# Optimization experiments

Hardware: AMD Instinct MI355X
Metric: run time of the kernel (lower is better)

Reference implementation:

```python
import jax, jax.numpy as jnp
import numpy as np

N = 100000
E = 500000
D_IN = 128
D_H = 128
MAX_ITERS = 3  # min(int(T=2.0)+1, 3); step weights all >= 0.5 so no early break


def setup_inputs() -> dict:
    key = jax.random.key(0)
    ks = jax.random.split(key, 7)
    node_feats = jax.random.normal(ks[0], (N, D_IN), dtype=jnp.float32)
    edge_index = jax.random.randint(ks[1], (2, E), 0, N, dtype=jnp.int64)
    init = lambda k, shp, fan: jax.random.normal(k, shp, dtype=jnp.float32) / np.float32(np.sqrt(fan))
    W_s = init(ks[2], (D_H, D_IN), D_IN)        # Linear(d_in, d_h, bias=False)
    W_pc = init(ks[3], (D_H, D_H), D_H)         # Linear(d_h, d_h, bias=False)
    W_edge = init(ks[4], (D_H, 2 * D_H), 2 * D_H)  # Linear(2*d_h, d_h, bias=False)
    W_gate_w = init(ks[5], (1, 2 * D_H), 2 * D_H)  # Linear(2*d_h, 1)
    W_gate_b = jnp.zeros((1,), jnp.float32)
    T = jnp.float32(2.0)  # learnable iteration-count parameter, init tree_iterations
    return dict(node_feats=node_feats, edge_index=edge_index, W_s=W_s, W_pc=W_pc,
                W_edge=W_edge, W_gate_w=W_gate_w, W_gate_b=W_gate_b, T=T)


def _step(h, p_idx, c_idx, W_pc, W_edge, W_gate_w, W_gate_b):
    h_p = h[p_idx]                                   # [E, d_h] gather
    h_c = h[c_idx]                                   # [E, d_h] gather
    ec = jnp.concatenate([h_p, h_c], axis=1)         # [E, 2*d_h]
    msg = ec @ W_edge.T                              # edge projection
    alpha = jax.nn.sigmoid(ec @ W_gate_w.T + W_gate_b)  # [E, 1] gate
    msg = msg * alpha
    # scatter_add into both endpoints (symmetric aggregation)
    agg = jnp.zeros_like(h).at[p_idx].add(msg).at[c_idx].add(msg)
    new_h = jax.nn.relu(agg @ W_pc.T + h)
    return new_h + h  # residual=True


def reference(node_feats, edge_index, W_s, W_pc, W_edge, W_gate_w, W_gate_b, T):
    p_idx, c_idx = edge_index[0], edge_index[1]
    h = node_feats @ W_s.T                           # [N, d_h]
    for step in range(MAX_ITERS):
        w = jax.nn.sigmoid(T - step)                 # learned step weight
        step_h = _step(h, p_idx, c_idx, W_pc, W_edge, W_gate_w, W_gate_b)
        h = h + w * (step_h - h)
    return h  # outputs['hidden'] (dropout is identity in eval)
```

## Files before the change

### kernel.cpp

```cpp
#include <hip/hip_runtime.h>
#include <cstdio>
#include <cstddef>

#define DH 128

typedef _Float16 f16;
typedef __attribute__((ext_vector_type(8))) _Float16 f16x8;
typedef __attribute__((ext_vector_type(4))) _Float16 f16x4;
typedef __attribute__((ext_vector_type(2))) _Float16 f16x2;
typedef __attribute__((ext_vector_type(4))) float    f32x4;
typedef unsigned int u32;

__global__ __launch_bounds__(128) void prep2(const float* __restrict__ Wpc,
                                             const float* __restrict__ Wedge,
                                             const float* __restrict__ Ws,
                                             f16* __restrict__ Bg16,
                                             f16* __restrict__ Ws16,
                                             const int* __restrict__ idx,
                                             int* __restrict__ cnt, int twoE)
{
    int o = blockIdx.x;
    int k = threadIdx.x;
    if (o < 256) {
        int orow = o & 127;
        int col  = (o < 128) ? k : (128 + k);
        float acc = 0.f;
        for (int m = 0; m < 128; ++m)
            acc += Wpc[orow * 128 + m] * Wedge[m * 256 + col];
        Bg16[o * 128 + k] = (f16)acc;
    } else if (o < 384) {
        int row = o - 256;
        Ws16[row * 128 + k] = (f16)Ws[row * 128 + k];
    } else {
        const int stride = (gridDim.x - 384) * 128;
        for (int i = (o - 384) * 128 + k; i < twoE; i += stride)
            atomicAdd(cnt + idx[i], 1);
    }
}

template<int OUT, int NT, bool AF32, bool WF32, bool WF16, bool FUSES>
__global__ __launch_bounds__(256) void mfma_gemm_t(const void* __restrict__ Avp,
                                                   const f16* __restrict__ B16,
                                                   float* __restrict__ Cf,
                                                   f16* __restrict__ Ch,
                                                   const float* __restrict__ wg,
                                                   float* __restrict__ s,
                                                   int M)
{
    const int lane = threadIdx.x & 63;
    const int row0 = blockIdx.x * (NT * 64) + (threadIdx.x >> 6) * (NT * 16);
    const int r = lane & 15, kg = lane >> 4;

    int  mrow[NT];
    bool ok[NT];
    f16x8 a[NT][4];
#pragma unroll
    for (int t = 0; t < NT; ++t) {
        mrow[t] = row0 + t * 16 + r;
        ok[t]   = (mrow[t] < M);
        int ar  = ok[t] ? mrow[t] : M - 1;
        if constexpr (AF32) {
            const float4* Ap = (const float4*)((const float*)Avp + (size_t)ar * 128);
#pragma unroll
            for (int q = 0; q < 4; ++q) {
                float4 f0 = Ap[kg * 2 + q * 8];
                float4 f1 = Ap[kg * 2 + q * 8 + 1];
                f16x8 fr = {(f16)f0.x, (f16)f0.y, (f16)f0.z, (f16)f0.w,
                            (f16)f1.x, (f16)f1.y, (f16)f1.z, (f16)f1.w};
                a[t][q] = fr;
            }
        } else {
            const f16x8* Ap = (const f16x8*)((const f16*)Avp + (size_t)ar * 128 + kg * 8);
            a[t][0] = Ap[0]; a[t][1] = Ap[4]; a[t][2] = Ap[8]; a[t][3] = Ap[12];
        }
    }

    float sp0[NT], sp1[NT];
    if constexpr (FUSES) {
#pragma unroll
        for (int t = 0; t < NT; ++t) { sp0[t] = 0.f; sp1[t] = 0.f; }
    }

    for (int ct = 0; ct < OUT / 16; ++ct) {
        const f16x8* Bp = (const f16x8*)(B16 + (size_t)(ct * 16 + r) * 128 + kg * 8);
        f16x8 b0 = Bp[0], b1 = Bp[4], b2 = Bp[8], b3 = Bp[12];
        const int o0 = ct * 16 + kg * 4;
        float w0, w1, w2, w3, u0, u1, u2, u3;
        if constexpr (FUSES) {
            w0 = wg[o0]; w1 = wg[o0+1]; w2 = wg[o0+2]; w3 = wg[o0+3];
            u0 = wg[128+o0]; u1 = wg[128+o0+1]; u2 = wg[128+o0+2]; u3 = wg[128+o0+3];
        }
#pragma unroll
        for (int t = 0; t < NT; ++t) {
            f32x4 acc = {0.f, 0.f, 0.f, 0.f};
            acc = __builtin_amdgcn_mfma_f32_16x16x32_f16(b0, a[t][0], acc, 0, 0, 0);
            acc = __builtin_amdgcn_mfma_f32_16x16x32_f16(b1, a[t][1], acc, 0, 0, 0);
            acc = __builtin_amdgcn_mfma_f32_16x16x32_f16(b2, a[t][2], acc, 0, 0, 0);
            acc = __builtin_amdgcn_mfma_f32_16x16x32_f16(b3, a[t][3], acc, 0, 0, 0);
            if (ok[t]) {
                if constexpr (WF32)
                    *(float4*)(Cf + (size_t)mrow[t] * OUT + o0) =
                        make_float4(acc[0], acc[1], acc[2], acc[3]);
                if constexpr (WF16) {
                    f16x4 hv = {(f16)acc[0], (f16)acc[1], (f16)acc[2], (f16)acc[3]};
                    *(f16x4*)(Ch + (size_t)mrow[t] * OUT + o0) = hv;
                }
            }
            if constexpr (FUSES) {
                sp0[t] += acc[0]*w0 + acc[1]*w1 + acc[2]*w2 + acc[3]*w3;
                sp1[t] += acc[0]*u0 + acc[1]*u1 + acc[2]*u2 + acc[3]*u3;
            }
        }
    }
    if constexpr (FUSES) {
#pragma unroll
        for (int t = 0; t < NT; ++t) {
            float p0 = sp0[t], p1 = sp1[t];
            p0 += __shfl_xor(p0, 16); p0 += __shfl_xor(p0, 32);
            p1 += __shfl_xor(p1, 16); p1 += __shfl_xor(p1, 32);
            if (kg == 0 && ok[t])
                *(float2*)(s + 2 * mrow[t]) = make_float2(p0, p1);
        }
    }
}

#define SCAN_B 256
__global__ __launch_bounds__(SCAN_B) void scan1(const int* __restrict__ cnt,
                                                int* __restrict__ bsum, int Nn)
{
    __shared__ int sm[SCAN_B];
    int i = blockIdx.x * SCAN_B + threadIdx.x;
    sm[threadIdx.x] = (i < Nn) ? cnt[i] : 0;
    __syncthreads();
    for (int off = SCAN_B / 2; off > 0; off >>= 1) {
        if (threadIdx.x < off) sm[threadIdx.x] += sm[threadIdx.x + off];
        __syncthreads();
    }
    if (threadIdx.x == 0) bsum[blockIdx.x] = sm[0];
}

__global__ __launch_bounds__(1024) void scan2(int* __restrict__ bsum, int nb,
                                              int* __restrict__ totalOut)
{
    __shared__ int sm[1024];
    int t = threadIdx.x;
    sm[t] = (t < nb) ? bsum[t] : 0;
    __syncthreads();
    for (int off = 1; off < 1024; off <<= 1) {
        int u = (t >= off) ? sm[t - off] : 0;
        __syncthreads();
        sm[t] += u;
        __syncthreads();
    }
    if (t < nb) bsum[t] = (t == 0) ? 0 : sm[t - 1];
    if (t == nb - 1) *totalOut = sm[t];
}

__global__ __launch_bounds__(SCAN_B) void scan3(const int* __restrict__ cnt,
                                                const int* __restrict__ bsum,
                                                int* __restrict__ base,
                                                int* __restrict__ cursor, int Nn)
{
    __shared__ int sm[SCAN_B];
    int i = blockIdx.x * SCAN_B + threadIdx.x;
    int v = (i < Nn) ? cnt[i] : 0;
    sm[threadIdx.x] = v;
    __syncthreads();
    for (int off = 1; off < SCAN_B; off <<= 1) {
        int u = (threadIdx.x >= off) ? sm[threadIdx.x - off] : 0;
        __syncthreads();
        sm[threadIdx.x] += u;
        __syncthreads();
    }
    if (i < Nn) {
        int b = bsum[blockIdx.x] + sm[threadIdx.x] - v;
        base[i] = b;
        cursor[i] = b;
    }
}

__global__ __launch_bounds__(256) void fill_xcd(const int* __restrict__ idx,
                                                int* __restrict__ cursor,
                                                int* __restrict__ adjp,
                                                int E, int Nn)
{
    const int xcd  = blockIdx.x & 7;
    const int gblk = blockIdx.x >> 3;
    const int ngrp = gridDim.x >> 3;
    const int twoE = 2 * E;
    const int lo = xcd * Nn, hi = lo + Nn;
    for (int i = gblk * blockDim.x + threadIdx.x; i < twoE; i += ngrp * blockDim.x) {
        int node = idx[i];
        int n8 = node << 3;
        if (n8 < lo || n8 >= hi) continue;
        int side  = (i >= E);
        int e     = side ? i - E : i;
        int other = side ? idx[e] : idx[E + e];
        int pos = atomicAdd(cursor + node, 1);
        adjp[pos] = other | (side << 31);
    }
}

template<bool LAST>
__global__ __launch_bounds__(256) void agg8(const f16* __restrict__ g16,
                                            const int* __restrict__ adjp,
                                            const int* __restrict__ base,
                                            const float* __restrict__ sIn,
                                            float* __restrict__ sOut,
                                            float* __restrict__ hOut,
                                            f16* __restrict__ h16,
                                            const float* __restrict__ wg,
                                            const float* __restrict__ gbp,
                                            const float* __restrict__ Tp,
                                            float stepf, int Nn, int twoE)
{
    const int lane = threadIdx.x & 63;
    const int grp  = lane >> 4;
    const int gl   = lane & 15;
    const int wvid = (blockIdx.x * blockDim.x + threadIdx.x) >> 6;
    int n = wvid * 4 + grp;
    const bool nOK = (n < Nn);
    if (n >= Nn) n = Nn - 1;
    const float gb = gbp[0];
    const float w  = 1.f / (1.f + expf(-(Tp[0] - stepf)));
    const int b0 = base[n], b1 = base[n + 1];
    const int deg = b1 - b0;
    const float s1n = sIn[2 * n], s2n = sIn[2 * n + 1];
    const int d0 = gl << 3;

    f16x8 o1 = *(const f16x8*)(g16 + (size_t)n * 256 + d0);
    f16x8 o2 = *(const f16x8*)(g16 + (size_t)n * 256 + 128 + d0);
    f16x8 hv16 = *(const f16x8*)(h16 + (size_t)n * DH + d0);

    f16x2 acc0 = {(f16)0.f, (f16)0.f};
    f16x2 acc1 = {(f16)0.f, (f16)0.f};
    f16x2 acc2 = {(f16)0.f, (f16)0.f};
    f16x2 acc3 = {(f16)0.f, (f16)0.f};
    float aPl = 0.f, aCl = 0.f;

    union V8 { f16x8 v; f16x2 h2[4]; };
    union AU { u32 w; f16x2 h; unsigned short us[2]; };

    int t = 0;
    while (__any(t * 16 < deg)) {
        const int done = t * 16;
        int m = deg - done; m = (m < 0) ? 0 : ((m > 16) ? 16 : m);
        int midx = b0 + done + ((gl < m) ? gl : ((m > 0) ? m - 1 : 0));
        midx = (midx < twoE - 1) ? midx : (twoE - 1);
        midx = (midx > 0) ? midx : 0;
        int meta  = adjp[midx];
        int other = meta & 0x7FFFFFFF;
        int side  = ((unsigned)meta) >> 31;
        int eoff  = (other << 8) | ((side ^ 1) << 7);
        float sv  = sIn[2 * other + (side ^ 1)];
        float aE  = 1.f / (1.f + expf(-((side ? s2n : s1n) + sv + gb)));
        if (gl >= m) aE = 0.f;
        aPl += side ? 0.f : aE;
        aCl += side ? aE : 0.f;

        AU apk;
        apk.h[0] = (f16)aE;
        apk.us[1] = apk.us[0];

        const int sb = grp << 4;
        for (int j = 0; j < m; j += 8) {
            V8 gv[8]; u32 ap[8];
#pragma unroll
            for (int u = 0; u < 8; ++u) {
                int es = j + u; es = (es < 15) ? es : 15;
                int eo = __shfl(eoff, sb | es);
                ap[u]  = (u32)__shfl((int)apk.w, sb | es);
                gv[u].v = *(const f16x8*)(g16 + (size_t)(unsigned)eo + d0);
            }
#pragma unroll
            for (int u = 0; u < 8; ++u) {
                AU aa; aa.w = ap[u];
                acc0 += aa.h * gv[u].h2[0];
                acc1 += aa.h * gv[u].h2[1];
                acc2 += aa.h * gv[u].h2[2];
                acc3 += aa.h * gv[u].h2[3];
            }
        }
        ++t;
    }

    float a8[8];
    a8[0] = (float)acc0[0]; a8[1] = (float)acc0[1];
    a8[2] = (float)acc1[0]; a8[3] = (float)acc1[1];
    a8[4] = (float)acc2[0]; a8[5] = (float)acc2[1];
    a8[6] = (float)acc3[0]; a8[7] = (float)acc3[1];

    float aP = aPl, aC = aCl;
#pragma unroll
    for (int off = 8; off > 0; off >>= 1) {
        aP += __shfl_xor(aP, off);
        aC += __shfl_xor(aC, off);
    }
#pragma unroll
    for (int i = 0; i < 8; ++i)
        a8[i] += aP * (float)o1[i] + aC * (float)o2[i];

    float hf[8];
#pragma unroll
    for (int i = 0; i < 8; ++i) {
        hf[i] = (float)hv16[i];
        hf[i] += w * fmaxf(a8[i] + hf[i], 0.f);
    }

    float p0 = 0.f, p1 = 0.f;
    if (nOK) {
        if constexpr (LAST) {
            *(float4*)(hOut + (size_t)n * DH + d0) =
                make_float4(hf[0], hf[1], hf[2], hf[3]);
            *(float4*)(hOut + (size_t)n * DH + d0 + 4) =
                make_float4(hf[4], hf[5], hf[6], hf[7]);
        } else {
            f16x8 h2 = {(f16)hf[0], (f16)hf[1], (f16)hf[2], (f16)hf[3],
                        (f16)hf[4], (f16)hf[5], (f16)hf[6], (f16)hf[7]};
            *(f16x8*)(h16 + (size_t)n * DH + d0) = h2;
        }
    }
    if constexpr (!LAST) {
        float4 w0a = *(const float4*)(wg + d0);
        float4 w0b = *(const float4*)(wg + d0 + 4);
        float4 w1a = *(const float4*)(wg + 128 + d0);
        float4 w1b = *(const float4*)(wg + 128 + d0 + 4);
        p0 = hf[0]*w0a.x + hf[1]*w0a.y + hf[2]*w0a.z + hf[3]*w0a.w
           + hf[4]*w0b.x + hf[5]*w0b.y + hf[6]*w0b.z + hf[7]*w0b.w;
        p1 = hf[0]*w1a.x + hf[1]*w1a.y + hf[2]*w1a.z + hf[3]*w1a.w
           + hf[4]*w1b.x + hf[5]*w1b.y + hf[6]*w1b.z + hf[7]*w1b.w;
#pragma unroll
        for (int off = 8; off > 0; off >>= 1) {
            p0 += __shfl_xor(p0, off);
            p1 += __shfl_xor(p1, off);
        }
        if (gl == 0 && nOK) *(float2*)(sOut + 2 * n) = make_float2(p0, p1);
    }
}

static inline size_t alignUp(size_t x) { return (x + 255) & ~(size_t)255; }

extern "C" void kernel_launch(void* const* d_in, const int* in_sizes, int n_in,
                              void* d_out, int out_size, void* d_ws, size_t ws_size,
                              hipStream_t stream)
{
    const float* x     = (const float*)d_in[0];
    const int*   idx   = (const int*)d_in[1];
    const float* Ws    = (const float*)d_in[2];
    const float* Wpc   = (const float*)d_in[3];
    const float* Wedge = (const float*)d_in[4];
    const float* Wg    = (const float*)d_in[5];
    const float* Wgb   = (const float*)d_in[6];
    const float* Tp    = (const float*)d_in[7];
    const int Nn = in_sizes[0] / DH;
    const int E  = in_sizes[1] / 2;
    float* h = (float*)d_out;

    const int nb = (Nn + SCAN_B - 1) / SCAN_B;
    if (nb > 1024) { fprintf(stderr, "kernel_launch: Nn too big for scan\n"); return; }

    size_t off = 0;
    char* wsb = (char*)d_ws;
    f16*   g16    = (f16*)  (wsb + off); off = alignUp(off + (size_t)Nn * 256 * 2);
    f16*   h16    = (f16*)  (wsb + off); off = alignUp(off + (size_t)Nn * DH * 2);
    f16*   Ws16   = (f16*)  (wsb + off); off = alignUp(off + 128 * 128 * 2);
    f16*   Bg16   = (f16*)  (wsb + off); off = alignUp(off + 256 * 128 * 2);
    float* sA     = (float*)(wsb + off); off = alignUp(off + (size_t)Nn * 2 * 4);
    float* sB     = (float*)(wsb + off); off = alignUp(off + (size_t)Nn * 2 * 4);
    int*   cnt    = (int*)  (wsb + off); off = alignUp(off + (size_t)Nn * 4);
    int*   base   = (int*)  (wsb + off); off = alignUp(off + (size_t)(Nn + 1) * 4);
    int*   cursor = (int*)  (wsb + off); off = alignUp(off + (size_t)Nn * 4);
    int*   bsum   = (int*)  (wsb + off); off = alignUp(off + 1024 * 4);
    int*   adjp   = (int*)  (wsb + off); off = alignUp(off + (size_t)(2 * E + 64) * 4);
    if (off > ws_size) {
        fprintf(stderr, "kernel_launch: ws too small (%zu < %zu)\n", ws_size, off);
        return;
    }

    hipMemsetAsync(cnt, 0, (size_t)Nn * 4, stream);
    prep2<<<dim3(2048), dim3(128), 0, stream>>>(Wpc, Wedge, Ws, Bg16, Ws16,
                                                idx, cnt, 2 * E);
    scan1<<<dim3(nb), dim3(SCAN_B), 0, stream>>>(cnt, bsum, Nn);
    scan2<<<dim3(1), dim3(1024), 0, stream>>>(bsum, nb, base + Nn);
    scan3<<<dim3(nb), dim3(SCAN_B), 0, stream>>>(cnt, bsum, base, cursor, Nn);
    fill_xcd<<<dim3(1280), dim3(256), 0, stream>>>(idx, cursor, adjp, E, Nn);

    mfma_gemm_t<128, 2, true, false, true, true>
        <<<dim3((Nn + 127) / 128), dim3(256), 0, stream>>>(x, Ws16, nullptr, h16,
                                                           Wg, sA, Nn);

    const int aggBlocks = (Nn * 16 + 255) / 256;
    float* sCur = sA; float* sNxt = sB;
    for (int step = 0; step < 3; ++step) {
        mfma_gemm_t<256, 4, false, false, true, false>
            <<<dim3((Nn + 255) / 256), dim3(256), 0, stream>>>(h16, Bg16, nullptr, g16,
                                                               nullptr, nullptr, Nn);
        if (step < 2)
            agg8<false><<<dim3(aggBlocks), dim3(256), 0, stream>>>(g16, adjp, base, sCur,
                                                                   sNxt, h, h16, Wg, Wgb,
                                                                   Tp, (float)step, Nn, 2 * E);
        else
            agg8<true><<<dim3(aggBlocks), dim3(256), 0, stream>>>(g16, adjp, base, sCur,
                                                                  sNxt, h, h16, Wg, Wgb,
                                                                  Tp, (float)step, Nn, 2 * E);
        float* t = sCur; sCur = sNxt; sNxt = t;
    }
}
```

Measured before the change: 385.1 us.

## Fuse setup kernels into heterogeneous megakernels and collapse scan passes

Edge counting, the combined-weight precompute and the initial projection GEMM (now reading fp32 W_s directly) are merged into one launch partitioned by block index. The CSR fill is co-scheduled with the first step's edge GEMM in a second launch. The three-pass scan becomes two passes, with each block summing its own prefix of block totals. The aim is to cut launch count and overlap independent setup work, at the cost of redundant prefix summation and mixed-workload blocks competing for resources.

```diff
diff --git a/kernel.cpp b/kernel.cpp
--- a/kernel.cpp
+++ b/kernel.cpp
@@ -11,44 +11,18 @@
 typedef __attribute__((ext_vector_type(4))) float    f32x4;
 typedef unsigned int u32;
 
-__global__ __launch_bounds__(128) void prep2(const float* __restrict__ Wpc,
-                                             const float* __restrict__ Wedge,
-                                             const float* __restrict__ Ws,
-                                             f16* __restrict__ Bg16,
-                                             f16* __restrict__ Ws16,
-                                             const int* __restrict__ idx,
-                                             int* __restrict__ cnt, int twoE)
-{
-    int o = blockIdx.x;
-    int k = threadIdx.x;
-    if (o < 256) {
-        int orow = o & 127;
-        int col  = (o < 128) ? k : (128 + k);
-        float acc = 0.f;
-        for (int m = 0; m < 128; ++m)
-            acc += Wpc[orow * 128 + m] * Wedge[m * 256 + col];
-        Bg16[o * 128 + k] = (f16)acc;
-    } else if (o < 384) {
-        int row = o - 256;
-        Ws16[row * 128 + k] = (f16)Ws[row * 128 + k];
-    } else {
-        const int stride = (gridDim.x - 384) * 128;
-        for (int i = (o - 384) * 128 + k; i < twoE; i += stride)
-            atomicAdd(cnt + idx[i], 1);
-    }
-}
-
-template<int OUT, int NT, bool AF32, bool WF32, bool WF16, bool FUSES>
-__global__ __launch_bounds__(256) void mfma_gemm_t(const void* __restrict__ Avp,
-                                                   const f16* __restrict__ B16,
-                                                   float* __restrict__ Cf,
-                                                   f16* __restrict__ Ch,
-                                                   const float* __restrict__ wg,
-                                                   float* __restrict__ s,
-                                                   int M)
-{
-    const int lane = threadIdx.x & 63;
-    const int row0 = blockIdx.x * (NT * 64) + (threadIdx.x >> 6) * (NT * 16);
+template<int OUT, int NT, bool AF32, bool BF32, bool WF32, bool WF16, bool FUSES>
+__device__ __forceinline__ void gemm_body(int bx, int tid,
+                                          const void* __restrict__ Avp,
+                                          const void* __restrict__ Bvp,
+                                          float* __restrict__ Cf,
+                                          f16* __restrict__ Ch,
+                                          const float* __restrict__ wg,
+                                          float* __restrict__ s,
+                                          int M)
+{
+    const int lane = tid & 63;
+    const int row0 = bx * (NT * 64) + (tid >> 6) * (NT * 16);
     const int r = lane & 15, kg = lane >> 4;
 
     int  mrow[NT];
@@ -60,11 +34,11 @@
         ok[t]   = (mrow[t] < M);
         int ar  = ok[t] ? mrow[t] : M - 1;
         if constexpr (AF32) {
-            const float4* Ap = (const float4*)((const float*)Avp + (size_t)ar * 128);
+            const float* Af = (const float*)Avp + (size_t)ar * 128 + kg * 8;
 #pragma unroll
             for (int q = 0; q < 4; ++q) {
-                float4 f0 = Ap[kg * 2 + q * 8];
-                float4 f1 = Ap[kg * 2 + q * 8 + 1];
+                float4 f0 = *(const float4*)(Af + q * 32);
+                float4 f1 = *(const float4*)(Af + q * 32 + 4);
                 f16x8 fr = {(f16)f0.x, (f16)f0.y, (f16)f0.z, (f16)f0.w,
                             (f16)f1.x, (f16)f1.y, (f16)f1.z, (f16)f1.w};
                 a[t][q] = fr;
@@ -82,8 +56,24 @@
     }
 
     for (int ct = 0; ct < OUT / 16; ++ct) {
-        const f16x8* Bp = (const f16x8*)(B16 + (size_t)(ct * 16 + r) * 128 + kg * 8);
-        f16x8 b0 = Bp[0], b1 = Bp[4], b2 = Bp[8], b3 = Bp[12];
+        f16x8 b0, b1, b2, b3;
+        if constexpr (BF32) {
+            const float* Bf = (const float*)Bvp + (size_t)(ct * 16 + r) * 128 + kg * 8;
+            f16x8 bq[4];
+#pragma unroll
+            for (int q = 0; q < 4; ++q) {
+                float4 f0 = *(const float4*)(Bf + q * 32);
+                float4 f1 = *(const float4*)(Bf + q * 32 + 4);
+                f16x8 fr = {(f16)f0.x, (f16)f0.y, (f16)f0.z, (f16)f0.w,
+                            (f16)f1.x, (f16)f1.y, (f16)f1.z, (f16)f1.w};
+                bq[q] = fr;
+            }
+            b0 = bq[0]; b1 = bq[1]; b2 = bq[2]; b3 = bq[3];
+        } else {
+            const f16x8* Bp = (const f16x8*)((const f16*)Bvp +
+                                             (size_t)(ct * 16 + r) * 128 + kg * 8);
+            b0 = Bp[0]; b1 = Bp[4]; b2 = Bp[8]; b3 = Bp[12];
+        }
         const int o0 = ct * 16 + kg * 4;
         float w0, w1, w2, w3, u0, u1, u2, u3;
         if constexpr (FUSES) {
@@ -124,6 +114,80 @@
     }
 }
 
+#define CNT_B 512
+__global__ __launch_bounds__(256) void megaA(const float* __restrict__ x,
+                                             const float* __restrict__ Ws,
+                                             const float* __restrict__ Wpc,
+                                             const float* __restrict__ Wedge,
+                                             f16* __restrict__ Bg16,
+                                             const int* __restrict__ idx,
+                                             int* __restrict__ cnt, int twoE,
+                                             const float* __restrict__ wg,
+                                             float* __restrict__ s,
+                                             f16* __restrict__ h16, int M)
+{
+    const int b = blockIdx.x;
+    if (b < CNT_B) {
+        const int stride = CNT_B * 256;
+        for (int i = b * 256 + threadIdx.x; i < twoE; i += stride)
+            atomicAdd(cnt + idx[i], 1);
+    } else if (b < CNT_B + 128) {
+        int ob = (b - CNT_B) * 2 + (threadIdx.x >> 7);
+        int k  = threadIdx.x & 127;
+        int orow = ob & 127;
+        int col  = (ob < 128) ? k : (128 + k);
+        float acc = 0.f;
+        for (int m = 0; m < 128; ++m)
+            acc += Wpc[orow * 128 + m] * Wedge[m * 256 + col];
+        Bg16[ob * 128 + k] = (f16)acc;
+    } else {
+        gemm_body<128, 2, true, true, false, true, true>(b - CNT_B - 128, threadIdx.x,
+                                                         x, Ws, nullptr, h16, wg, s, M);
+    }
+}
+
+#define FILL_B 1280
+__global__ __launch_bounds__(256) void megaB(const int* __restrict__ idx,
+                                             int* __restrict__ cursor,
+                                             int* __restrict__ adjp,
+                                             int E, int Nn,
+                                             const f16* __restrict__ h16,
+                                             const f16* __restrict__ Bg16,
+                                             f16* __restrict__ g16, int M)
+{
+    const int b = blockIdx.x;
+    if (b < FILL_B) {
+        const int xcd  = b & 7;
+        const int gblk = b >> 3;
+        const int ngrp = FILL_B >> 3;
+        const int twoE = 2 * E;
+        const int lo = xcd * Nn, hi = lo + Nn;
+        for (int i = gblk * blockDim.x + threadIdx.x; i < twoE; i += ngrp * blockDim.x) {
+            int node = idx[i];
+            int n8 = node << 3;
+            if (n8 < lo || n8 >= hi) continue;
+            int side  = (i >= E);
+            int e     = side ? i - E : i;
+            int other = side ? idx[e] : idx[E + e];
+            int pos = atomicAdd(cursor + node, 1);
+            adjp[pos] = other | (side << 31);
+        }
+    } else {
+        gemm_body<256, 4, false, false, false, true, false>(b - FILL_B, threadIdx.x,
+                                                            h16, Bg16, nullptr, g16,
+                                                            nullptr, nullptr, M);
+    }
+}
+
+__global__ __launch_bounds__(256) void gemm256(const f16* __restrict__ A16,
+                                               const f16* __restrict__ B16,
+                                               f16* __restrict__ Ch, int M)
+{
+    gemm_body<256, 4, false, false, false, true, false>(blockIdx.x, threadIdx.x,
+                                                        A16, B16, nullptr, Ch,
+                                                        nullptr, nullptr, M);
+}
+
 #define SCAN_B 256
 __global__ __launch_bounds__(SCAN_B) void scan1(const int* __restrict__ cnt,
                                                 int* __restrict__ bsum, int Nn)
@@ -139,29 +203,25 @@
     if (threadIdx.x == 0) bsum[blockIdx.x] = sm[0];
 }
 
-__global__ __launch_bounds__(1024) void scan2(int* __restrict__ bsum, int nb,
-                                              int* __restrict__ totalOut)
-{
-    __shared__ int sm[1024];
-    int t = threadIdx.x;
-    sm[t] = (t < nb) ? bsum[t] : 0;
+__global__ __launch_bounds__(SCAN_B) void scan3b(const int* __restrict__ cnt,
+                                                 const int* __restrict__ bsum,
+                                                 int* __restrict__ base,
+                                                 int* __restrict__ cursor, int Nn)
+{
+    __shared__ int sm[SCAN_B];
+    __shared__ int spre;
+    int acc = 0;
+    for (int t = threadIdx.x; t < blockIdx.x; t += SCAN_B) acc += bsum[t];
+    sm[threadIdx.x] = acc;
     __syncthreads();
-    for (int off = 1; off < 1024; off <<= 1) {
-        int u = (t >= off) ? sm[t - off] : 0;
+    for (int off = SCAN_B / 2; off > 0; off >>= 1) {
+        if (threadIdx.x < off) sm[threadIdx.x] += sm[threadIdx.x + off];
         __syncthreads();
-        sm[t] += u;
-        __syncthreads();
-    }
-    if (t < nb) bsum[t] = (t == 0) ? 0 : sm[t - 1];
-    if (t == nb - 1) *totalOut = sm[t];
-}
-
-__global__ __launch_bounds__(SCAN_B) void scan3(const int* __restrict__ cnt,
-                                                const int* __restrict__ bsum,
-                                                int* __restrict__ base,
-                                                int* __restrict__ cursor, int Nn)
-{
-    __shared__ int sm[SCAN_B];
+    }
+    if (threadIdx.x == 0) spre = sm[0];
+    __syncthreads();
+    const int bpre = spre;
+    __syncthreads();
     int i = blockIdx.x * SCAN_B + threadIdx.x;
     int v = (i < Nn) ? cnt[i] : 0;
     sm[threadIdx.x] = v;
@@ -173,31 +233,10 @@
         __syncthreads();
     }
     if (i < Nn) {
-        int b = bsum[blockIdx.x] + sm[threadIdx.x] - v;
+        int b = bpre + sm[threadIdx.x] - v;
         base[i] = b;
         cursor[i] = b;
-    }
-}
-
-__global__ __launch_bounds__(256) void fill_xcd(const int* __restrict__ idx,
-                                                int* __restrict__ cursor,
-                                                int* __restrict__ adjp,
-                                                int E, int Nn)
-{
-    const int xcd  = blockIdx.x & 7;
-    const int gblk = blockIdx.x >> 3;
-    const int ngrp = gridDim.x >> 3;
-    const int twoE = 2 * E;
-    const int lo = xcd * Nn, hi = lo + Nn;
-    for (int i = gblk * blockDim.x + threadIdx.x; i < twoE; i += ngrp * blockDim.x) {
-        int node = idx[i];
-        int n8 = node << 3;
-        if (n8 < lo || n8 >= hi) continue;
-        int side  = (i >= E);
-        int e     = side ? i - E : i;
-        int other = side ? idx[e] : idx[E + e];
-        int pos = atomicAdd(cursor + node, 1);
-        adjp[pos] = other | (side << 31);
+        if (i == Nn - 1) base[Nn] = b + v;
     }
 }
 
@@ -357,44 +396,42 @@
     float* h = (float*)d_out;
 
     const int nb = (Nn + SCAN_B - 1) / SCAN_B;
-    if (nb > 1024) { fprintf(stderr, "kernel_launch: Nn too big for scan\n"); return; }
 
     size_t off = 0;
     char* wsb = (char*)d_ws;
     f16*   g16    = (f16*)  (wsb + off); off = alignUp(off + (size_t)Nn * 256 * 2);
     f16*   h16    = (f16*)  (wsb + off); off = alignUp(off + (size_t)Nn * DH * 2);
-    f16*   Ws16   = (f16*)  (wsb + off); off = alignUp(off + 128 * 128 * 2);
     f16*   Bg16   = (f16*)  (wsb + off); off = alignUp(off + 256 * 128 * 2);
     float* sA     = (float*)(wsb + off); off = alignUp(off + (size_t)Nn * 2 * 4);
     float* sB     = (float*)(wsb + off); off = alignUp(off + (size_t)Nn * 2 * 4);
     int*   cnt    = (int*)  (wsb + off); off = alignUp(off + (size_t)Nn * 4);
     int*   base   = (int*)  (wsb + off); off = alignUp(off + (size_t)(Nn + 1) * 4);
     int*   cursor = (int*)  (wsb + off); off = alignUp(off + (size_t)Nn * 4);
-    int*   bsum   = (int*)  (wsb + off); off = alignUp(off + 1024 * 4);
+    int*   bsum   = (int*)  (wsb + off); off = alignUp(off + (size_t)(nb + 1) * 4);
     int*   adjp   = (int*)  (wsb + off); off = alignUp(off + (size_t)(2 * E + 64) * 4);
     if (off > ws_size) {
         fprintf(stderr, "kernel_launch: ws too small (%zu < %zu)\n", ws_size, off);
         return;
     }
 
+    const int gemmInitBlocks = (Nn + 127) / 128;
+    const int gemmStepBlocks = (Nn + 255) / 256;
+
     hipMemsetAsync(cnt, 0, (size_t)Nn * 4, stream);
-    prep2<<<dim3(2048), dim3(128), 0, stream>>>(Wpc, Wedge, Ws, Bg16, Ws16,
-                                                idx, cnt, 2 * E);
+    megaA<<<dim3(CNT_B + 128 + gemmInitBlocks), dim3(256), 0, stream>>>(
+        x, Ws, Wpc, Wedge, Bg16, idx, cnt, 2 * E, Wg, sA, h16, Nn);
+
     scan1<<<dim3(nb), dim3(SCAN_B), 0, stream>>>(cnt, bsum, Nn);
-    scan2<<<dim3(1), dim3(1024), 0, stream>>>(bsum, nb, base + Nn);
-    scan3<<<dim3(nb), dim3(SCAN_B), 0, stream>>>(cnt, bsum, base, cursor, Nn);
-    fill_xcd<<<dim3(1280), dim3(256), 0, stream>>>(idx, cursor, adjp, E, Nn);
-
-    mfma_gemm_t<128, 2, true, false, true, true>
-        <<<dim3((Nn + 127) / 128), dim3(256), 0, stream>>>(x, Ws16, nullptr, h16,
-                                                           Wg, sA, Nn);
+    scan3b<<<dim3(nb), dim3(SCAN_B), 0, stream>>>(cnt, bsum, base, cursor, Nn);
+
+    megaB<<<dim3(FILL_B + gemmStepBlocks), dim3(256), 0, stream>>>(
+        idx, cursor, adjp, E, Nn, h16, Bg16, g16, Nn);
 
     const int aggBlocks = (Nn * 16 + 255) / 256;
     float* sCur = sA; float* sNxt = sB;
     for (int step = 0; step < 3; ++step) {
-        mfma_gemm_t<256, 4, false, false, true, false>
-            <<<dim3((Nn + 255) / 256), dim3(256), 0, stream>>>(h16, Bg16, nullptr, g16,
-                                                               nullptr, nullptr, Nn);
+        if (step > 0)
+            gemm256<<<dim3(gemmStepBlocks), dim3(256), 0, stream>>>(h16, Bg16, g16, Nn);
         if (step < 2)
             agg8<false><<<dim3(aggBlocks), dim3(256), 0, stream>>>(g16, adjp, base, sCur,
                                                                    sNxt, h, h16, Wg, Wgb,
```

Measured after the change: 397.9 us. 1.03x slower.
